# Kernel tuning notes

Hardware: AMD Instinct MI355X
Metric: run time of the kernel (lower is better)

## Reference

```python
import jax, jax.numpy as jnp
import numpy as np

B, N, T, D, O = 8, 1024, 12, 64, 64

def setup_inputs() -> dict:
    key = jax.random.key(0)
    k1, k2, k3 = jax.random.split(key, 3)
    x = jax.random.normal(k1, (B, N, T, D), dtype=jnp.float32)
    # row-normalized random adjacency (dense mask, as in the torch module)
    adj = jax.random.uniform(k2, (N, N), dtype=jnp.float32)
    norm_adj = adj / jnp.sum(adj, axis=-1, keepdims=True)
    theta_w = jax.random.normal(k3, (D, O), dtype=jnp.float32) / np.sqrt(D)
    return {"x": x, "norm_adj": norm_adj, "theta_w": theta_w}

def reference(x, norm_adj, theta_w):
    b, n, t, d = x.shape
    # [B, N, T, D] -> [B*T, N, D]
    xr = jnp.transpose(x, (0, 2, 1, 3)).reshape(b * t, n, d)
    # spatial attention scores [B*T, N, N]
    scores = jnp.einsum('gnd,gmd->gnm', xr, xr) / jnp.sqrt(jnp.float32(d))
    attn = jax.nn.softmax(scores, axis=-1)
    # adjacency-masked attention, then aggregate and project
    agg = jnp.einsum('gnm,gmd->gnd', norm_adj[None, :, :] * attn, xr)
    out = jnp.einsum('gnd,do->gno', agg, theta_w)
    # [B*T, N, O] -> [B, N, T, O], relu
    out = jnp.transpose(out.reshape(b, t, n, -1), (0, 2, 1, 3))
    return jax.nn.relu(out)
```

## Files before the change

kernel.cpp:

```cpp
#include <hip/hip_runtime.h>


#define NB    8
#define NT    12
#define NNODE 1024
#define ND    64
#define XROW  768

typedef __bf16 bf16x8 __attribute__((ext_vector_type(8)));
typedef float  floatx4 __attribute__((ext_vector_type(4)));

#define MFMA(a,b,c) __builtin_amdgcn_mfma_f32_16x16x32_bf16((a),(b),(c),0,0,0)

#define QSCALE 0.18033688011112042f

#define KSTRIDE 72
#define VSTRIDE 40
#define PSTRIDE 36
#define AGSTRIDE 68
#define OFF_KHI 0
#define OFF_KLO 4608
#define OFF_VHI 9216
#define OFF_VLO 14336
#define OFF_P   19456
#define SMEM_BYTES (19456 + 128*PSTRIDE*4)

struct bfpair { __bf16 h, l; };

__device__ __forceinline__ bfpair split1(float f) {
    bfpair r;
    __bf16 hb = (__bf16)f;
    float hf = __builtin_bit_cast(float,
                   (unsigned)__builtin_bit_cast(unsigned short, hb) << 16);
    r.h = hb;
    r.l = (__bf16)(f - hf);
    return r;
}

__global__ void __launch_bounds__(256, 2)
spattn(const float* __restrict__ x, const float* __restrict__ adj,
       const float* __restrict__ theta, float* __restrict__ out)
{
    __shared__ __align__(16) char smem[SMEM_BYTES];
    __bf16* Khi = (__bf16*)(smem + OFF_KHI);
    __bf16* Klo = (__bf16*)(smem + OFF_KLO);
    __bf16* Vhi = (__bf16*)(smem + OFF_VHI);
    __bf16* Vlo = (__bf16*)(smem + OFF_VLO);
    float*  Pm  = (float*)(smem + OFF_P);

    const int tid  = threadIdx.x;
    const int wave = tid >> 6;
    const int lane = tid & 63;
    const int l16  = lane & 15;
    const int quad = lane >> 4;

    const int bx   = blockIdx.x;
    const int g    = bx >> 3;
    const int rblk = bx & 7;
    const int bb   = g / NT;
    const int tt   = g - bb * NT;
    const int row0 = rblk * 128;

    const float* xbase = x + (size_t)bb * (NNODE * XROW) + tt * ND;

    bf16x8 qhi[2][2], qlo[2][2];
    #pragma unroll
    for (int mt = 0; mt < 2; ++mt) {
        const float* qsrc = xbase + (size_t)(row0 + wave*32 + mt*16 + l16) * XROW;
        #pragma unroll
        for (int ks = 0; ks < 2; ++ks) {
            floatx4 f0 = *(const floatx4*)(qsrc + ks*32 + quad*8);
            floatx4 f1 = *(const floatx4*)(qsrc + ks*32 + quad*8 + 4);
            #pragma unroll
            for (int i = 0; i < 4; ++i) {
                bfpair p0 = split1(f0[i]*QSCALE);
                qhi[mt][ks][i]   = p0.h; qlo[mt][ks][i]   = p0.l;
                bfpair p1 = split1(f1[i]*QSCALE);
                qhi[mt][ks][4+i] = p1.h; qlo[mt][ks][4+i] = p1.l;
            }
        }
    }

    const floatx4 vzero = {0.f, 0.f, 0.f, 0.f};
    floatx4 acc[2][4];
    #pragma unroll
    for (int mt = 0; mt < 2; ++mt)
        #pragma unroll
        for (int dt = 0; dt < 4; ++dt)
            acc[mt][dt] = vzero;
    float lpart[2][4] = {{0.f,0.f,0.f,0.f},{0.f,0.f,0.f,0.f}};

    const int skey = tid >> 3;
    const int sd0  = (tid & 7) * 8;
    const int svd  = tid >> 2;
    const int svk0 = (tid & 3) * 8;
    floatx4 kf0, kf1;
    float vf[8];

    {
        const float* ksrc = xbase + (size_t)skey * XROW + sd0;
        kf0 = *(const floatx4*)ksrc;
        kf1 = *(const floatx4*)(ksrc + 4);
        const float* vsrc = xbase + (size_t)svk0 * XROW + svd;
        #pragma unroll
        for (int i = 0; i < 8; ++i) vf[i] = vsrc[i * XROW];
    }

    for (int ct = 0; ct < 32; ++ct) {
        const int key0 = ct * 32;
        __syncthreads();
        {
            bf16x8 h, l;
            #pragma unroll
            for (int i = 0; i < 4; ++i) {
                bfpair p0 = split1(kf0[i]); h[i]   = p0.h; l[i]   = p0.l;
                bfpair p1 = split1(kf1[i]); h[4+i] = p1.h; l[4+i] = p1.l;
            }
            *(bf16x8*)(Khi + skey*KSTRIDE + sd0) = h;
            *(bf16x8*)(Klo + skey*KSTRIDE + sd0) = l;
            bf16x8 vh, vl;
            #pragma unroll
            for (int i = 0; i < 8; ++i) {
                bfpair p = split1(vf[i]); vh[i] = p.h; vl[i] = p.l;
            }
            *(bf16x8*)(Vhi + svd*VSTRIDE + svk0) = vh;
            *(bf16x8*)(Vlo + svd*VSTRIDE + svk0) = vl;
        }
        __syncthreads();
        if (ct < 31) {
            const int nk = key0 + 32;
            const float* ksrc = xbase + (size_t)(nk + skey) * XROW + sd0;
            kf0 = *(const floatx4*)ksrc;
            kf1 = *(const floatx4*)(ksrc + 4);
            const float* vsrc = xbase + (size_t)(nk + svk0) * XROW + svd;
            #pragma unroll
            for (int i = 0; i < 8; ++i) vf[i] = vsrc[i * XROW];
        }
        float av[2][2][4];
        #pragma unroll
        for (int mt = 0; mt < 2; ++mt)
            #pragma unroll
            for (int nt = 0; nt < 2; ++nt)
                #pragma unroll
                for (int r = 0; r < 4; ++r)
                    av[mt][nt][r] = adj[(size_t)(row0 + wave*32 + mt*16 + quad*4 + r) * NNODE
                                        + key0 + nt*16 + l16];

        floatx4 S[2][2] = {{vzero, vzero}, {vzero, vzero}};
        #pragma unroll
        for (int ks = 0; ks < 2; ++ks) {
            #pragma unroll
            for (int nt = 0; nt < 2; ++nt) {
                bf16x8 bh = *(const bf16x8*)(Khi + (nt*16 + l16)*KSTRIDE + ks*32 + quad*8);
                bf16x8 bl = *(const bf16x8*)(Klo + (nt*16 + l16)*KSTRIDE + ks*32 + quad*8);
                #pragma unroll
                for (int mt = 0; mt < 2; ++mt) {
                    S[mt][nt] = MFMA(qhi[mt][ks], bh, S[mt][nt]);
                    S[mt][nt] = MFMA(qlo[mt][ks], bh, S[mt][nt]);
                    S[mt][nt] = MFMA(qhi[mt][ks], bl, S[mt][nt]);
                }
            }
        }
        #pragma unroll
        for (int mt = 0; mt < 2; ++mt)
            #pragma unroll
            for (int nt = 0; nt < 2; ++nt)
                #pragma unroll
                for (int r = 0; r < 4; ++r) {
                    float w = __builtin_amdgcn_exp2f(S[mt][nt][r]);
                    lpart[mt][r] += w;
                    Pm[(wave*32 + mt*16 + quad*4 + r)*PSTRIDE + nt*16 + l16] = av[mt][nt][r] * w;
                }
        bf16x8 pah[2], pal[2];
        #pragma unroll
        for (int mt = 0; mt < 2; ++mt) {
            const float* pp = Pm + (wave*32 + mt*16 + l16)*PSTRIDE + quad*8;
            floatx4 p0 = *(const floatx4*)pp;
            floatx4 p1 = *(const floatx4*)(pp + 4);
            #pragma unroll
            for (int i = 0; i < 4; ++i) {
                bfpair q0 = split1(p0[i]); pah[mt][i]   = q0.h; pal[mt][i]   = q0.l;
                bfpair q1 = split1(p1[i]); pah[mt][4+i] = q1.h; pal[mt][4+i] = q1.l;
            }
        }
        #pragma unroll
        for (int dt = 0; dt < 4; ++dt) {
            bf16x8 vh = *(const bf16x8*)(Vhi + (dt*16 + l16)*VSTRIDE + quad*8);
            bf16x8 vl = *(const bf16x8*)(Vlo + (dt*16 + l16)*VSTRIDE + quad*8);
            #pragma unroll
            for (int mt = 0; mt < 2; ++mt) {
                acc[mt][dt] = MFMA(pah[mt], vh, acc[mt][dt]);
                acc[mt][dt] = MFMA(pal[mt], vh, acc[mt][dt]);
                acc[mt][dt] = MFMA(pah[mt], vl, acc[mt][dt]);
            }
        }
    }

    float linv[2][4];
    #pragma unroll
    for (int mt = 0; mt < 2; ++mt)
        #pragma unroll
        for (int r = 0; r < 4; ++r) {
            float lv = lpart[mt][r];
            lv += __shfl_xor(lv, 1);
            lv += __shfl_xor(lv, 2);
            lv += __shfl_xor(lv, 4);
            lv += __shfl_xor(lv, 8);
            linv[mt][r] = 1.0f / lv;
        }

    __syncthreads();
    float* AG = (float*)smem;
    #pragma unroll
    for (int mt = 0; mt < 2; ++mt)
        #pragma unroll
        for (int dt = 0; dt < 4; ++dt)
            #pragma unroll
            for (int r = 0; r < 4; ++r)
                AG[(wave*32 + mt*16 + quad*4 + r)*AGSTRIDE + dt*16 + l16]
                    = acc[mt][dt][r] * linv[mt][r];

    bf16x8 th[4][2], tl[4][2];
    #pragma unroll
    for (int ot = 0; ot < 4; ++ot)
        #pragma unroll
        for (int ks = 0; ks < 2; ++ks)
            #pragma unroll
            for (int j = 0; j < 8; ++j) {
                float tv = theta[(ks*32 + quad*8 + j)*ND + ot*16 + l16];
                bfpair p = split1(tv);
                th[ot][ks][j] = p.h; tl[ot][ks][j] = p.l;
            }

    floatx4 oacc[2][4];
    #pragma unroll
    for (int mt = 0; mt < 2; ++mt)
        #pragma unroll
        for (int ot = 0; ot < 4; ++ot)
            oacc[mt][ot] = vzero;
    __syncthreads();
    #pragma unroll
    for (int ks = 0; ks < 2; ++ks) {
        bf16x8 ah[2], al[2];
        #pragma unroll
        for (int mt = 0; mt < 2; ++mt) {
            const float* ap = AG + (wave*32 + mt*16 + l16)*AGSTRIDE + ks*32 + quad*8;
            floatx4 a0 = *(const floatx4*)ap;
            floatx4 a1 = *(const floatx4*)(ap + 4);
            #pragma unroll
            for (int i = 0; i < 4; ++i) {
                bfpair q0 = split1(a0[i]); ah[mt][i]   = q0.h; al[mt][i]   = q0.l;
                bfpair q1 = split1(a1[i]); ah[mt][4+i] = q1.h; al[mt][4+i] = q1.l;
            }
        }
        #pragma unroll
        for (int ot = 0; ot < 4; ++ot)
            #pragma unroll
            for (int mt = 0; mt < 2; ++mt) {
                oacc[mt][ot] = MFMA(ah[mt], th[ot][ks], oacc[mt][ot]);
                oacc[mt][ot] = MFMA(al[mt], th[ot][ks], oacc[mt][ot]);
                oacc[mt][ot] = MFMA(ah[mt], tl[ot][ks], oacc[mt][ot]);
            }
    }

    float* obase = out + (size_t)bb * (NNODE * XROW) + tt * ND;
    #pragma unroll
    for (int mt = 0; mt < 2; ++mt)
        #pragma unroll
        for (int ot = 0; ot < 4; ++ot)
            #pragma unroll
            for (int r = 0; r < 4; ++r) {
                float v = oacc[mt][ot][r];
                obase[(size_t)(row0 + wave*32 + mt*16 + quad*4 + r) * XROW + ot*16 + l16]
                    = v > 0.f ? v : 0.f;
            }
}

extern "C" void kernel_launch(void* const* d_in, const int* in_sizes, int n_in,
                              void* d_out, int out_size, void* d_ws, size_t ws_size,
                              hipStream_t stream) {
    (void)in_sizes; (void)n_in; (void)d_ws; (void)ws_size; (void)out_size;
    const float* x     = (const float*)d_in[0];
    const float* adj   = (const float*)d_in[1];
    const float* theta = (const float*)d_in[2];
    float* out = (float*)d_out;
    spattn<<<dim3(768), dim3(256), 0, stream>>>(x, adj, theta, out);
}
```

Before: 173.3 us.

## Use 512-thread blocks with 16 query rows per wave and split K/V staging

The block grows from 4 to 8 waves. Each wave now owns one 16-row query tile instead of two, which roughly halves the accumulators, Q fragments and S tiles held in registers. K and V staging is divided between the two halves of the block, so each thread converts and stores only K or only V per key tile. The launch-bounds hint rises to 512 threads with 6 blocks per SM to push occupancy up. The cost is that each wave now reuses its K/V LDS fragments across one M-tile instead of two, so LDS reads per MFMA roughly double, and barriers now span more waves.

```diff
diff --git a/kernel.cpp b/kernel.cpp
--- a/kernel.cpp
+++ b/kernel.cpp
@@ -37,7 +37,7 @@
     return r;
 }
 
-__global__ void __launch_bounds__(256, 2)
+__global__ void __launch_bounds__(512, 6)
 spattn(const float* __restrict__ x, const float* __restrict__ adj,
        const float* __restrict__ theta, float* __restrict__ out)
 {
@@ -63,10 +63,9 @@
 
     const float* xbase = x + (size_t)bb * (NNODE * XROW) + tt * ND;
 
-    bf16x8 qhi[2][2], qlo[2][2];
-    #pragma unroll
-    for (int mt = 0; mt < 2; ++mt) {
-        const float* qsrc = xbase + (size_t)(row0 + wave*32 + mt*16 + l16) * XROW;
+    bf16x8 qhi[2], qlo[2];
+    {
+        const float* qsrc = xbase + (size_t)(row0 + wave*16 + l16) * XROW;
         #pragma unroll
         for (int ks = 0; ks < 2; ++ks) {
             floatx4 f0 = *(const floatx4*)(qsrc + ks*32 + quad*8);
@@ -74,33 +73,33 @@
             #pragma unroll
             for (int i = 0; i < 4; ++i) {
                 bfpair p0 = split1(f0[i]*QSCALE);
-                qhi[mt][ks][i]   = p0.h; qlo[mt][ks][i]   = p0.l;
+                qhi[ks][i]   = p0.h; qlo[ks][i]   = p0.l;
                 bfpair p1 = split1(f1[i]*QSCALE);
-                qhi[mt][ks][4+i] = p1.h; qlo[mt][ks][4+i] = p1.l;
+                qhi[ks][4+i] = p1.h; qlo[ks][4+i] = p1.l;
             }
         }
     }
 
     const floatx4 vzero = {0.f, 0.f, 0.f, 0.f};
-    floatx4 acc[2][4];
-    #pragma unroll
-    for (int mt = 0; mt < 2; ++mt)
-        #pragma unroll
-        for (int dt = 0; dt < 4; ++dt)
-            acc[mt][dt] = vzero;
-    float lpart[2][4] = {{0.f,0.f,0.f,0.f},{0.f,0.f,0.f,0.f}};
-
-    const int skey = tid >> 3;
-    const int sd0  = (tid & 7) * 8;
-    const int svd  = tid >> 2;
-    const int svk0 = (tid & 3) * 8;
+    floatx4 acc[4];
+    #pragma unroll
+    for (int dt = 0; dt < 4; ++dt) acc[dt] = vzero;
+    float lpart[4] = {0.f, 0.f, 0.f, 0.f};
+
+    const int half = tid >> 8;
+    const int htid = tid & 255;
+    const int skey = htid >> 3;
+    const int sd0  = (htid & 7) * 8;
+    const int svd  = htid >> 2;
+    const int svk0 = (htid & 3) * 8;
     floatx4 kf0, kf1;
     float vf[8];
 
-    {
+    if (half == 0) {
         const float* ksrc = xbase + (size_t)skey * XROW + sd0;
         kf0 = *(const floatx4*)ksrc;
         kf1 = *(const floatx4*)(ksrc + 4);
+    } else {
         const float* vsrc = xbase + (size_t)svk0 * XROW + svd;
         #pragma unroll
         for (int i = 0; i < 8; ++i) vf[i] = vsrc[i * XROW];
@@ -109,7 +108,7 @@
     for (int ct = 0; ct < 32; ++ct) {
         const int key0 = ct * 32;
         __syncthreads();
-        {
+        if (half == 0) {
             bf16x8 h, l;
             #pragma unroll
             for (int i = 0; i < 4; ++i) {
@@ -118,6 +117,7 @@
             }
             *(bf16x8*)(Khi + skey*KSTRIDE + sd0) = h;
             *(bf16x8*)(Klo + skey*KSTRIDE + sd0) = l;
+        } else {
             bf16x8 vh, vl;
             #pragma unroll
             for (int i = 0; i < 8; ++i) {
@@ -129,96 +129,84 @@
         __syncthreads();
         if (ct < 31) {
             const int nk = key0 + 32;
-            const float* ksrc = xbase + (size_t)(nk + skey) * XROW + sd0;
-            kf0 = *(const floatx4*)ksrc;
-            kf1 = *(const floatx4*)(ksrc + 4);
-            const float* vsrc = xbase + (size_t)(nk + svk0) * XROW + svd;
-            #pragma unroll
-            for (int i = 0; i < 8; ++i) vf[i] = vsrc[i * XROW];
-        }
-        float av[2][2][4];
-        #pragma unroll
-        for (int mt = 0; mt < 2; ++mt)
-            #pragma unroll
-            for (int nt = 0; nt < 2; ++nt)
+            if (half == 0) {
+                const float* ksrc = xbase + (size_t)(nk + skey) * XROW + sd0;
+                kf0 = *(const floatx4*)ksrc;
+                kf1 = *(const floatx4*)(ksrc + 4);
+            } else {
+                const float* vsrc = xbase + (size_t)(nk + svk0) * XROW + svd;
                 #pragma unroll
-                for (int r = 0; r < 4; ++r)
-                    av[mt][nt][r] = adj[(size_t)(row0 + wave*32 + mt*16 + quad*4 + r) * NNODE
-                                        + key0 + nt*16 + l16];
-
-        floatx4 S[2][2] = {{vzero, vzero}, {vzero, vzero}};
+                for (int i = 0; i < 8; ++i) vf[i] = vsrc[i * XROW];
+            }
+        }
+        float av[2][4];
+        #pragma unroll
+        for (int nt = 0; nt < 2; ++nt)
+            #pragma unroll
+            for (int r = 0; r < 4; ++r)
+                av[nt][r] = adj[(size_t)(row0 + wave*16 + quad*4 + r) * NNODE
+                                + key0 + nt*16 + l16];
+
+        floatx4 S[2] = {vzero, vzero};
         #pragma unroll
         for (int ks = 0; ks < 2; ++ks) {
             #pragma unroll
             for (int nt = 0; nt < 2; ++nt) {
                 bf16x8 bh = *(const bf16x8*)(Khi + (nt*16 + l16)*KSTRIDE + ks*32 + quad*8);
                 bf16x8 bl = *(const bf16x8*)(Klo + (nt*16 + l16)*KSTRIDE + ks*32 + quad*8);
-                #pragma unroll
-                for (int mt = 0; mt < 2; ++mt) {
-                    S[mt][nt] = MFMA(qhi[mt][ks], bh, S[mt][nt]);
-                    S[mt][nt] = MFMA(qlo[mt][ks], bh, S[mt][nt]);
-                    S[mt][nt] = MFMA(qhi[mt][ks], bl, S[mt][nt]);
-                }
-            }
-        }
-        #pragma unroll
-        for (int mt = 0; mt < 2; ++mt)
-            #pragma unroll
-            for (int nt = 0; nt < 2; ++nt)
-                #pragma unroll
-                for (int r = 0; r < 4; ++r) {
-                    float w = __builtin_amdgcn_exp2f(S[mt][nt][r]);
-                    lpart[mt][r] += w;
-                    Pm[(wave*32 + mt*16 + quad*4 + r)*PSTRIDE + nt*16 + l16] = av[mt][nt][r] * w;
-                }
-        bf16x8 pah[2], pal[2];
-        #pragma unroll
-        for (int mt = 0; mt < 2; ++mt) {
-            const float* pp = Pm + (wave*32 + mt*16 + l16)*PSTRIDE + quad*8;
+                S[nt] = MFMA(qhi[ks], bh, S[nt]);
+                S[nt] = MFMA(qlo[ks], bh, S[nt]);
+                S[nt] = MFMA(qhi[ks], bl, S[nt]);
+            }
+        }
+        #pragma unroll
+        for (int nt = 0; nt < 2; ++nt)
+            #pragma unroll
+            for (int r = 0; r < 4; ++r) {
+                float w = __builtin_amdgcn_exp2f(S[nt][r]);
+                lpart[r] += w;
+                Pm[(wave*16 + quad*4 + r)*PSTRIDE + nt*16 + l16] = av[nt][r] * w;
+            }
+        bf16x8 pah, pal;
+        {
+            const float* pp = Pm + (wave*16 + l16)*PSTRIDE + quad*8;
             floatx4 p0 = *(const floatx4*)pp;
             floatx4 p1 = *(const floatx4*)(pp + 4);
             #pragma unroll
             for (int i = 0; i < 4; ++i) {
-                bfpair q0 = split1(p0[i]); pah[mt][i]   = q0.h; pal[mt][i]   = q0.l;
-                bfpair q1 = split1(p1[i]); pah[mt][4+i] = q1.h; pal[mt][4+i] = q1.l;
+                bfpair q0 = split1(p0[i]); pah[i]   = q0.h; pal[i]   = q0.l;
+                bfpair q1 = split1(p1[i]); pah[4+i] = q1.h; pal[4+i] = q1.l;
             }
         }
         #pragma unroll
         for (int dt = 0; dt < 4; ++dt) {
             bf16x8 vh = *(const bf16x8*)(Vhi + (dt*16 + l16)*VSTRIDE + quad*8);
             bf16x8 vl = *(const bf16x8*)(Vlo + (dt*16 + l16)*VSTRIDE + quad*8);
-            #pragma unroll
-            for (int mt = 0; mt < 2; ++mt) {
-                acc[mt][dt] = MFMA(pah[mt], vh, acc[mt][dt]);
-                acc[mt][dt] = MFMA(pal[mt], vh, acc[mt][dt]);
-                acc[mt][dt] = MFMA(pah[mt], vl, acc[mt][dt]);
-            }
-        }
-    }
-
-    float linv[2][4];
-    #pragma unroll
-    for (int mt = 0; mt < 2; ++mt)
-        #pragma unroll
-        for (int r = 0; r < 4; ++r) {
-            float lv = lpart[mt][r];
-            lv += __shfl_xor(lv, 1);
-            lv += __shfl_xor(lv, 2);
-            lv += __shfl_xor(lv, 4);
-            lv += __shfl_xor(lv, 8);
-            linv[mt][r] = 1.0f / lv;
-        }
+            acc[dt] = MFMA(pah, vh, acc[dt]);
+            acc[dt] = MFMA(pal, vh, acc[dt]);
+            acc[dt] = MFMA(pah, vl, acc[dt]);
+        }
+    }
+
+    float linv[4];
+    #pragma unroll
+    for (int r = 0; r < 4; ++r) {
+        float lv = lpart[r];
+        lv += __shfl_xor(lv, 1);
+        lv += __shfl_xor(lv, 2);
+        lv += __shfl_xor(lv, 4);
+        lv += __shfl_xor(lv, 8);
+        linv[r] = 1.0f / lv;
+    }
 
     __syncthreads();
     float* AG = (float*)smem;
     #pragma unroll
-    for (int mt = 0; mt < 2; ++mt)
-        #pragma unroll
-        for (int dt = 0; dt < 4; ++dt)
-            #pragma unroll
-            for (int r = 0; r < 4; ++r)
-                AG[(wave*32 + mt*16 + quad*4 + r)*AGSTRIDE + dt*16 + l16]
-                    = acc[mt][dt][r] * linv[mt][r];
+    for (int dt = 0; dt < 4; ++dt)
+        #pragma unroll
+        for (int r = 0; r < 4; ++r)
+            AG[(wave*16 + quad*4 + r)*AGSTRIDE + dt*16 + l16]
+                = acc[dt][r] * linv[r];
 
     bf16x8 th[4][2], tl[4][2];
     #pragma unroll
@@ -232,48 +220,40 @@
                 th[ot][ks][j] = p.h; tl[ot][ks][j] = p.l;
             }
 
-    floatx4 oacc[2][4];
-    #pragma unroll
-    for (int mt = 0; mt < 2; ++mt)
-        #pragma unroll
-        for (int ot = 0; ot < 4; ++ot)
-            oacc[mt][ot] = vzero;
+    floatx4 oacc[4];
+    #pragma unroll
+    for (int ot = 0; ot < 4; ++ot) oacc[ot] = vzero;
     __syncthreads();
     #pragma unroll
     for (int ks = 0; ks < 2; ++ks) {
-        bf16x8 ah[2], al[2];
-        #pragma unroll
-        for (int mt = 0; mt < 2; ++mt) {
-            const float* ap = AG + (wave*32 + mt*16 + l16)*AGSTRIDE + ks*32 + quad*8;
+        bf16x8 ah, al;
+        {
+            const float* ap = AG + (wave*16 + l16)*AGSTRIDE + ks*32 + quad*8;
             floatx4 a0 = *(const floatx4*)ap;
             floatx4 a1 = *(const floatx4*)(ap + 4);
             #pragma unroll
             for (int i = 0; i < 4; ++i) {
-                bfpair q0 = split1(a0[i]); ah[mt][i]   = q0.h; al[mt][i]   = q0.l;
-                bfpair q1 = split1(a1[i]); ah[mt][4+i] = q1.h; al[mt][4+i] = q1.l;
-            }
-        }
-        #pragma unroll
-        for (int ot = 0; ot < 4; ++ot)
-            #pragma unroll
-            for (int mt = 0; mt < 2; ++mt) {
-                oacc[mt][ot] = MFMA(ah[mt], th[ot][ks], oacc[mt][ot]);
-                oacc[mt][ot] = MFMA(al[mt], th[ot][ks], oacc[mt][ot]);
-                oacc[mt][ot] = MFMA(ah[mt], tl[ot][ks], oacc[mt][ot]);
-            }
+                bfpair q0 = split1(a0[i]); ah[i]   = q0.h; al[i]   = q0.l;
+                bfpair q1 = split1(a1[i]); ah[4+i] = q1.h; al[4+i] = q1.l;
+            }
+        }
+        #pragma unroll
+        for (int ot = 0; ot < 4; ++ot) {
+            oacc[ot] = MFMA(ah, th[ot][ks], oacc[ot]);
+            oacc[ot] = MFMA(al, th[ot][ks], oacc[ot]);
+            oacc[ot] = MFMA(ah, tl[ot][ks], oacc[ot]);
+        }
     }
 
     float* obase = out + (size_t)bb * (NNODE * XROW) + tt * ND;
     #pragma unroll
-    for (int mt = 0; mt < 2; ++mt)
-        #pragma unroll
-        for (int ot = 0; ot < 4; ++ot)
-            #pragma unroll
-            for (int r = 0; r < 4; ++r) {
-                float v = oacc[mt][ot][r];
-                obase[(size_t)(row0 + wave*32 + mt*16 + quad*4 + r) * XROW + ot*16 + l16]
-                    = v > 0.f ? v : 0.f;
-            }
+    for (int ot = 0; ot < 4; ++ot)
+        #pragma unroll
+        for (int r = 0; r < 4; ++r) {
+            float v = oacc[ot][r];
+            obase[(size_t)(row0 + wave*16 + quad*4 + r) * XROW + ot*16 + l16]
+                = v > 0.f ? v : 0.f;
+        }
 }
 
 extern "C" void kernel_launch(void* const* d_in, const int* in_sizes, int n_in,
@@ -284,5 +264,5 @@
     const float* adj   = (const float*)d_in[1];
     const float* theta = (const float*)d_in[2];
     float* out = (float*)d_out;
-    spattn<<<dim3(768), dim3(256), 0, stream>>>(x, adj, theta, out);
+    spattn<<<dim3(768), dim3(512), 0, stream>>>(x, adj, theta, out);
 }
```

Result: slower. 295.6 us (+70.6%).

## Presplit x and theta into bf16 hi/lo workspace, then run smaller-tile attention kernel

Applied to the files above, without the earlier changes.

Adds a pre-pass kernel that splits x (row-major and transposed) and theta into bf16 hi/lo pairs in the workspace once per group. The main kernel then streams pre-split bf16 tiles instead of converting fp32 in every block. It also halves the row tile to 64 rows per block, doubles the grid, and raises the occupancy target. The aim is to remove redundant per-block split work and improve occupancy, at the cost of an extra launch and a large workspace write and read. The old kernel is kept as a fallback when the workspace is too small.

```diff
diff --git a/kernel.cpp b/kernel.cpp
--- a/kernel.cpp
+++ b/kernel.cpp
@@ -6,8 +6,10 @@
 #define NNODE 1024
 #define ND    64
 #define XROW  768
+#define NG    96
 
 typedef __bf16 bf16x8 __attribute__((ext_vector_type(8)));
+typedef __bf16 bf16x4 __attribute__((ext_vector_type(4)));
 typedef float  floatx4 __attribute__((ext_vector_type(4)));
 
 #define MFMA(a,b,c) __builtin_amdgcn_mfma_f32_16x16x32_bf16((a),(b),(c),0,0,0)
@@ -23,7 +25,16 @@
 #define OFF_VHI 9216
 #define OFF_VLO 14336
 #define OFF_P   19456
-#define SMEM_BYTES (19456 + 128*PSTRIDE*4)
+#define SMEM2   (19456 + 64*PSTRIDE*4)
+#define SMEM_FB (19456 + 128*PSTRIDE*4)
+
+#define WXHI  0
+#define WXLO  6291456
+#define WXTHI 12582912
+#define WXTLO 18874368
+#define WTHI  25165824
+#define WTLO  25169920
+#define WS_BYTES 50348032ULL
 
 struct bfpair { __bf16 h, l; };
 
@@ -37,11 +48,265 @@
     return r;
 }
 
+__global__ void __launch_bounds__(256)
+presplit(const float* __restrict__ x, const float* __restrict__ theta,
+         __bf16* __restrict__ ws)
+{
+    __shared__ __align__(16) float T[64 * 68];
+    const int tid  = threadIdx.x;
+    const int bx   = blockIdx.x;
+    const int g    = bx >> 4;
+    const int nblk = bx & 15;
+    const int bb   = g / NT;
+    const int tt   = g - bb * NT;
+    const int n0   = nblk * 64;
+
+    __bf16* Xhi  = ws + WXHI  + (size_t)g * 65536;
+    __bf16* Xlo  = ws + WXLO  + (size_t)g * 65536;
+    __bf16* XThi = ws + WXTHI + (size_t)g * 65536;
+    __bf16* XTlo = ws + WXTLO + (size_t)g * 65536;
+    const float* xg = x + (size_t)bb * (NNODE * XROW) + (size_t)tt * ND;
+
+    #pragma unroll
+    for (int i = 0; i < 4; ++i) {
+        int chunk = i * 256 + tid;
+        int n  = chunk >> 4;
+        int c4 = (chunk & 15) * 4;
+        floatx4 f = *(const floatx4*)(xg + (size_t)(n0 + n) * XROW + c4);
+        *(floatx4*)(T + n * 68 + c4) = f;
+        bf16x4 h, l;
+        #pragma unroll
+        for (int j = 0; j < 4; ++j) {
+            bfpair p = split1(f[j]); h[j] = p.h; l[j] = p.l;
+        }
+        *(bf16x4*)(Xhi + (size_t)(n0 + n) * 64 + c4) = h;
+        *(bf16x4*)(Xlo + (size_t)(n0 + n) * 64 + c4) = l;
+    }
+    __syncthreads();
+
+    {
+        const int d  = tid >> 2;
+        const int nc = (tid & 3) * 16;
+        bf16x8 h0, l0, h1, l1;
+        #pragma unroll
+        for (int j = 0; j < 8; ++j) {
+            bfpair p = split1(T[(nc + j) * 68 + d]);     h0[j] = p.h; l0[j] = p.l;
+            bfpair q = split1(T[(nc + 8 + j) * 68 + d]); h1[j] = q.h; l1[j] = q.l;
+        }
+        __bf16* dsth = XThi + (size_t)d * NNODE + n0 + nc;
+        __bf16* dstl = XTlo + (size_t)d * NNODE + n0 + nc;
+        *(bf16x8*)dsth = h0; *(bf16x8*)(dsth + 8) = h1;
+        *(bf16x8*)dstl = l0; *(bf16x8*)(dstl + 8) = l1;
+    }
+
+    if (bx < 2) {
+        int c  = bx * 256 + tid;
+        int o  = c >> 3;
+        int d0 = (c & 7) * 8;
+        bf16x8 h, l;
+        #pragma unroll
+        for (int i = 0; i < 8; ++i) {
+            bfpair p = split1(theta[(size_t)(d0 + i) * ND + o]);
+            h[i] = p.h; l[i] = p.l;
+        }
+        *(bf16x8*)(ws + WTHI + (size_t)o * 64 + d0) = h;
+        *(bf16x8*)(ws + WTLO + (size_t)o * 64 + d0) = l;
+    }
+}
+
+__global__ void __launch_bounds__(256, 5)
+spattn2(const __bf16* __restrict__ ws, const float* __restrict__ adj,
+        float* __restrict__ out)
+{
+    __shared__ __align__(16) char smem[SMEM2];
+    __bf16* Khi = (__bf16*)(smem + OFF_KHI);
+    __bf16* Klo = (__bf16*)(smem + OFF_KLO);
+    __bf16* Vhi = (__bf16*)(smem + OFF_VHI);
+    __bf16* Vlo = (__bf16*)(smem + OFF_VLO);
+    float*  Pm  = (float*)(smem + OFF_P);
+
+    const int tid  = threadIdx.x;
+    const int wave = tid >> 6;
+    const int lane = tid & 63;
+    const int l16  = lane & 15;
+    const int quad = lane >> 4;
+
+    const int bx   = blockIdx.x;
+    const int g    = bx >> 4;
+    const int rblk = bx & 15;
+    const int bb   = g / NT;
+    const int tt   = g - bb * NT;
+    const int row0 = rblk * 64;
+
+    const __bf16* xh  = ws + WXHI  + (size_t)g * 65536;
+    const __bf16* xl  = ws + WXLO  + (size_t)g * 65536;
+    const __bf16* xth = ws + WXTHI + (size_t)g * 65536;
+    const __bf16* xtl = ws + WXTLO + (size_t)g * 65536;
+
+    bf16x8 qhi[2], qlo[2];
+    {
+        const __bf16* q0 = xh + (size_t)(row0 + wave*16 + l16) * 64;
+        const __bf16* q1 = xl + (size_t)(row0 + wave*16 + l16) * 64;
+        #pragma unroll
+        for (int ks = 0; ks < 2; ++ks) {
+            qhi[ks] = *(const bf16x8*)(q0 + ks*32 + quad*8);
+            qlo[ks] = *(const bf16x8*)(q1 + ks*32 + quad*8);
+        }
+    }
+
+    const floatx4 vzero = {0.f, 0.f, 0.f, 0.f};
+    floatx4 acc[4];
+    #pragma unroll
+    for (int dt = 0; dt < 4; ++dt) acc[dt] = vzero;
+    float lpart[4] = {0.f, 0.f, 0.f, 0.f};
+
+    const int skey = tid >> 3;
+    const int sd0  = (tid & 7) * 8;
+    const int svd  = tid >> 2;
+    const int svk0 = (tid & 3) * 8;
+
+    bf16x8 kh, kl, pvh, pvl;
+    kh  = *(const bf16x8*)(xh  + (size_t)skey * 64 + sd0);
+    kl  = *(const bf16x8*)(xl  + (size_t)skey * 64 + sd0);
+    pvh = *(const bf16x8*)(xth + (size_t)svd * NNODE + svk0);
+    pvl = *(const bf16x8*)(xtl + (size_t)svd * NNODE + svk0);
+
+    for (int ct = 0; ct < 32; ++ct) {
+        const int key0 = ct * 32;
+        __syncthreads();
+        *(bf16x8*)(Khi + skey*KSTRIDE + sd0)  = kh;
+        *(bf16x8*)(Klo + skey*KSTRIDE + sd0)  = kl;
+        *(bf16x8*)(Vhi + svd*VSTRIDE + svk0)  = pvh;
+        *(bf16x8*)(Vlo + svd*VSTRIDE + svk0)  = pvl;
+        __syncthreads();
+        if (ct < 31) {
+            const int nk = key0 + 32;
+            kh  = *(const bf16x8*)(xh  + (size_t)(nk + skey) * 64 + sd0);
+            kl  = *(const bf16x8*)(xl  + (size_t)(nk + skey) * 64 + sd0);
+            pvh = *(const bf16x8*)(xth + (size_t)svd * NNODE + nk + svk0);
+            pvl = *(const bf16x8*)(xtl + (size_t)svd * NNODE + nk + svk0);
+        }
+        float av[2][4];
+        #pragma unroll
+        for (int nt = 0; nt < 2; ++nt)
+            #pragma unroll
+            for (int r = 0; r < 4; ++r)
+                av[nt][r] = adj[(size_t)(row0 + wave*16 + quad*4 + r) * NNODE
+                                + key0 + nt*16 + l16];
+
+        floatx4 S[2] = {vzero, vzero};
+        #pragma unroll
+        for (int ks = 0; ks < 2; ++ks) {
+            #pragma unroll
+            for (int nt = 0; nt < 2; ++nt) {
+                bf16x8 bh = *(const bf16x8*)(Khi + (nt*16 + l16)*KSTRIDE + ks*32 + quad*8);
+                bf16x8 bl = *(const bf16x8*)(Klo + (nt*16 + l16)*KSTRIDE + ks*32 + quad*8);
+                S[nt] = MFMA(qhi[ks], bh, S[nt]);
+                S[nt] = MFMA(qlo[ks], bh, S[nt]);
+                S[nt] = MFMA(qhi[ks], bl, S[nt]);
+            }
+        }
+        #pragma unroll
+        for (int nt = 0; nt < 2; ++nt)
+            #pragma unroll
+            for (int r = 0; r < 4; ++r) {
+                float w = __builtin_amdgcn_exp2f(S[nt][r] * QSCALE);
+                lpart[r] += w;
+                Pm[(wave*16 + quad*4 + r)*PSTRIDE + nt*16 + l16] = av[nt][r] * w;
+            }
+        bf16x8 pah, pal;
+        {
+            const float* pp = Pm + (wave*16 + l16)*PSTRIDE + quad*8;
+            floatx4 p0 = *(const floatx4*)pp;
+            floatx4 p1 = *(const floatx4*)(pp + 4);
+            #pragma unroll
+            for (int i = 0; i < 4; ++i) {
+                bfpair q0 = split1(p0[i]); pah[i]   = q0.h; pal[i]   = q0.l;
+                bfpair q1 = split1(p1[i]); pah[4+i] = q1.h; pal[4+i] = q1.l;
+            }
+        }
+        #pragma unroll
+        for (int dt = 0; dt < 4; ++dt) {
+            bf16x8 vvh = *(const bf16x8*)(Vhi + (dt*16 + l16)*VSTRIDE + quad*8);
+            bf16x8 vvl = *(const bf16x8*)(Vlo + (dt*16 + l16)*VSTRIDE + quad*8);
+            acc[dt] = MFMA(pah, vvh, acc[dt]);
+            acc[dt] = MFMA(pal, vvh, acc[dt]);
+            acc[dt] = MFMA(pah, vvl, acc[dt]);
+        }
+    }
+
+    float linv[4];
+    #pragma unroll
+    for (int r = 0; r < 4; ++r) {
+        float lv = lpart[r];
+        lv += __shfl_xor(lv, 1);
+        lv += __shfl_xor(lv, 2);
+        lv += __shfl_xor(lv, 4);
+        lv += __shfl_xor(lv, 8);
+        linv[r] = 1.0f / lv;
+    }
+
+    __syncthreads();
+    float* AG = (float*)smem;
+    #pragma unroll
+    for (int dt = 0; dt < 4; ++dt)
+        #pragma unroll
+        for (int r = 0; r < 4; ++r)
+            AG[(wave*16 + quad*4 + r)*AGSTRIDE + dt*16 + l16]
+                = acc[dt][r] * linv[r];
+
+    const __bf16* Th = ws + WTHI;
+    const __bf16* Tl = ws + WTLO;
+    bf16x8 th[4][2], tlw[4][2];
+    #pragma unroll
+    for (int ot = 0; ot < 4; ++ot)
+        #pragma unroll
+        for (int ks = 0; ks < 2; ++ks) {
+            th[ot][ks]  = *(const bf16x8*)(Th + (size_t)(ot*16 + l16)*64 + ks*32 + quad*8);
+            tlw[ot][ks] = *(const bf16x8*)(Tl + (size_t)(ot*16 + l16)*64 + ks*32 + quad*8);
+        }
+
+    floatx4 oacc[4];
+    #pragma unroll
+    for (int ot = 0; ot < 4; ++ot) oacc[ot] = vzero;
+    __syncthreads();
+    #pragma unroll
+    for (int ks = 0; ks < 2; ++ks) {
+        bf16x8 ah, al;
+        {
+            const float* ap = AG + (wave*16 + l16)*AGSTRIDE + ks*32 + quad*8;
+            floatx4 a0 = *(const floatx4*)ap;
+            floatx4 a1 = *(const floatx4*)(ap + 4);
+            #pragma unroll
+            for (int i = 0; i < 4; ++i) {
+                bfpair q0 = split1(a0[i]); ah[i]   = q0.h; al[i]   = q0.l;
+                bfpair q1 = split1(a1[i]); ah[4+i] = q1.h; al[4+i] = q1.l;
+            }
+        }
+        #pragma unroll
+        for (int ot = 0; ot < 4; ++ot) {
+            oacc[ot] = MFMA(ah, th[ot][ks], oacc[ot]);
+            oacc[ot] = MFMA(al, th[ot][ks], oacc[ot]);
+            oacc[ot] = MFMA(ah, tlw[ot][ks], oacc[ot]);
+        }
+    }
+
+    float* obase = out + (size_t)bb * (NNODE * XROW) + tt * ND;
+    #pragma unroll
+    for (int ot = 0; ot < 4; ++ot)
+        #pragma unroll
+        for (int r = 0; r < 4; ++r) {
+            float v = oacc[ot][r];
+            obase[(size_t)(row0 + wave*16 + quad*4 + r) * XROW + ot*16 + l16]
+                = v > 0.f ? v : 0.f;
+        }
+}
+
 __global__ void __launch_bounds__(256, 2)
-spattn(const float* __restrict__ x, const float* __restrict__ adj,
-       const float* __restrict__ theta, float* __restrict__ out)
+spattn_fb(const float* __restrict__ x, const float* __restrict__ adj,
+          const float* __restrict__ theta, float* __restrict__ out)
 {
-    __shared__ __align__(16) char smem[SMEM_BYTES];
+    __shared__ __align__(16) char smem[SMEM_FB];
     __bf16* Khi = (__bf16*)(smem + OFF_KHI);
     __bf16* Klo = (__bf16*)(smem + OFF_KLO);
     __bf16* Vhi = (__bf16*)(smem + OFF_VHI);
@@ -279,10 +544,16 @@
 extern "C" void kernel_launch(void* const* d_in, const int* in_sizes, int n_in,
                               void* d_out, int out_size, void* d_ws, size_t ws_size,
                               hipStream_t stream) {
-    (void)in_sizes; (void)n_in; (void)d_ws; (void)ws_size; (void)out_size;
+    (void)in_sizes; (void)n_in; (void)out_size;
     const float* x     = (const float*)d_in[0];
     const float* adj   = (const float*)d_in[1];
     const float* theta = (const float*)d_in[2];
     float* out = (float*)d_out;
-    spattn<<<dim3(768), dim3(256), 0, stream>>>(x, adj, theta, out);
+    if (d_ws != nullptr && ws_size >= WS_BYTES) {
+        __bf16* ws = (__bf16*)d_ws;
+        presplit<<<dim3(1536), dim3(256), 0, stream>>>(x, theta, ws);
+        spattn2<<<dim3(1536), dim3(256), 0, stream>>>(ws, adj, out);
+    } else {
+        spattn_fb<<<dim3(768), dim3(256), 0, stream>>>(x, adj, theta, out);
+    }
 }
```

New measurement: 213.7 us. 1.23x slower.
